# Kernel optimization log

Hardware: AMD Instinct MI355X
Metric: run time of the kernel (lower is better)

Reference implementation:

```python
import jax, jax.numpy as jnp
import numpy as np

D_IN, D_OUT, HEADS, D_K = 256, 256, 8, 32
B, N, L = 2, 128, 512
SCALING = 1.0 / np.sqrt(D_K)


def setup_inputs() -> dict:
    key = jax.random.key(0)
    ks = jax.random.split(key, 12)
    s = 0.02
    return {
        "query": jax.random.normal(ks[0], (B, L, D_IN), jnp.float32),
        "key": jax.random.normal(ks[1], (B, L, D_IN), jnp.float32),
        "value": jax.random.normal(ks[2], (B, N, L, D_OUT), jnp.float32),
        "mask": jax.random.uniform(ks[3], (B, 1, L, L), jnp.float32),
        "Wq": jax.random.normal(ks[4], (D_IN, HEADS * D_K), jnp.float32) * s,
        "bq": jnp.zeros((HEADS * D_K,), jnp.float32),
        "Wk": jax.random.normal(ks[5], (D_IN, HEADS * D_K), jnp.float32) * s,
        "bk": jnp.zeros((HEADS * D_K,), jnp.float32),
        "Wv": jax.random.normal(ks[6], (D_OUT, D_OUT), jnp.float32) * s,
        "bv": jnp.zeros((D_OUT,), jnp.float32),
        "Wo": jax.random.normal(ks[7], (D_OUT, D_OUT), jnp.float32) * s,
        "bo": jnp.zeros((D_OUT,), jnp.float32),
    }


def reference(query, key, value, mask, Wq, bq, Wk, bk, Wv, bv, Wo, bo):
    b, n, l = value.shape[:3]
    h, dk = HEADS, D_K
    dh = value.shape[-1] // h  # per-head value dim
    # projections -> per-head layouts
    q = (query @ Wq + bq).reshape(b, l, h, dk).transpose(0, 2, 1, 3)  # bhld
    k = (key @ Wk + bk).reshape(b, l, h, dk).transpose(0, 2, 1, 3)    # bhld
    v = (value @ Wv + bv).reshape(b, n, l, h, dh).transpose(0, 3, 1, 2, 4)  # bhnld
    q = q * SCALING
    scores = jnp.einsum('bhid,bhjd->bhij', q, k)  # (B,H,L,L)
    scores = jnp.where(mask < 0.5, jnp.finfo(scores.dtype).min, scores)
    attn = jax.nn.softmax(scores, axis=-1)
    # dropout omitted (eval mode / deterministic reference)
    out = jnp.einsum('bhij,bhnjd->bhnid', attn, v)  # (B,H,N,L,dh)
    out = out.transpose(0, 2, 3, 1, 4).reshape(b, n, l, h * dh)
    return out @ Wo + bo
```

## Files before the change

kernel.cpp:

```cpp
#include <hip/hip_runtime.h>
#include <hip/hip_bf16.h>
#include <stdint.h>

#define BB 2
#define LL 512
#define DIN 256
#define HH 8
#define DKK 32
#define NN 128
#define DM 256
#define SCALING 0.17677669529663687f

typedef unsigned short u16;
typedef float f32x4 __attribute__((ext_vector_type(4)));
typedef short s16x8 __attribute__((ext_vector_type(8)));

#define MFMA16(a, b, c) __builtin_amdgcn_mfma_f32_16x16x32_bf16((a), (b), (c), 0, 0, 0)

typedef __attribute__((address_space(3))) char lds_char;
typedef const __attribute__((address_space(1))) char glb_char;

__device__ __forceinline__ void gload16(const void* g, void* l) {
    __builtin_amdgcn_global_load_lds((glb_char*)g, (lds_char*)l, 16, 0, 0);
}

__device__ __forceinline__ u16 f2bf(float f) {
    union { float f; uint32_t i; } v; v.f = f;
    uint32_t x = v.i;
    return (u16)((x + 0x7fffu + ((x >> 16) & 1u)) >> 16);
}

__device__ __forceinline__ uint32_t pack2bf(float f0, float f1) {
    union { float f; uint32_t i; } a, b;
    a.f = f0; b.f = f1;
    return __builtin_amdgcn_perm(b.i + 0x8000u, a.i + 0x8000u, 0x07060302u);
}

__device__ __forceinline__ s16x8 ldsfrag(const u16* base, int row, int cb) {
    const char* p = (const char*)base + row * 128 + (cb ^ ((row & 7) << 4));
    return *(const s16x8*)(const void*)p;
}

__global__ __launch_bounds__(256) void prep_weights(
        const float* __restrict__ Wq, const float* __restrict__ Wk,
        const float* __restrict__ Wv, const float* __restrict__ Wo,
        u16* __restrict__ wqt, u16* __restrict__ wkt,
        u16* __restrict__ wvt, u16* __restrict__ wot) {
    int idx = blockIdx.x * 256 + threadIdx.x;
    int which = idx >> 16;
    const float* src = (which == 0) ? Wq : (which == 1) ? Wk : (which == 2) ? Wv : Wo;
    u16* dst = (which == 0) ? wqt : (which == 1) ? wkt : (which == 2) ? wvt : wot;
    int i = idx & 65535;
    int c = i & 255;
    int k = i >> 8;
    dst[(size_t)c * 256 + k] = f2bf(src[(size_t)k * 256 + c]);
}

__global__ __launch_bounds__(256) void qk_proj(
        const float* __restrict__ q_in, const float* __restrict__ k_in,
        const u16* __restrict__ wqt, const float* __restrict__ bq,
        const u16* __restrict__ wkt, const float* __restrict__ bk,
        u16* __restrict__ q_ws, u16* __restrict__ k_ws) {
    int bid = blockIdx.x;
    int isK = bid & 1;
    int r0 = (bid >> 1) * 64;
    const float* src = isK ? k_in : q_in;
    const u16* wt    = isK ? wkt : wqt;
    const float* bias = isK ? bk : bq;
    u16* dst = isK ? k_ws : q_ws;
    float scale = isK ? 1.0f : SCALING;

    int t = threadIdx.x, w = t >> 6, l = t & 63, lr = l & 15, lg = l >> 4;

    f32x4 zero = {0.f, 0.f, 0.f, 0.f};
    f32x4 acc[4][4];
#pragma unroll
    for (int m = 0; m < 4; m++)
#pragma unroll
        for (int cf = 0; cf < 4; cf++) acc[m][cf] = zero;

#pragma unroll
    for (int ks = 0; ks < 8; ks++) {
        s16x8 afr[4];
#pragma unroll
        for (int m = 0; m < 4; m++) {
            const float* p = src + (size_t)(r0 + m * 16 + lr) * DIN + ks * 32 + lg * 8;
            float4 v0 = *(const float4*)p;
            float4 v1 = *(const float4*)(p + 4);
            union { u16 u[8]; s16x8 v; } tmp;
            tmp.u[0] = f2bf(v0.x); tmp.u[1] = f2bf(v0.y);
            tmp.u[2] = f2bf(v0.z); tmp.u[3] = f2bf(v0.w);
            tmp.u[4] = f2bf(v1.x); tmp.u[5] = f2bf(v1.y);
            tmp.u[6] = f2bf(v1.z); tmp.u[7] = f2bf(v1.w);
            afr[m] = tmp.v;
        }
        s16x8 bfrg[4];
#pragma unroll
        for (int cf = 0; cf < 4; cf++)
            bfrg[cf] = *(const s16x8*)(const void*)(wt + (size_t)(w * 64 + cf * 16 + lr) * 256 + ks * 32 + lg * 8);
#pragma unroll
        for (int m = 0; m < 4; m++)
#pragma unroll
            for (int cf = 0; cf < 4; cf++) acc[m][cf] = MFMA16(afr[m], bfrg[cf], acc[m][cf]);
    }

#pragma unroll
    for (int m = 0; m < 4; m++)
#pragma unroll
        for (int cf = 0; cf < 4; cf++) {
            int c = w * 64 + cf * 16 + lr;
            int h = c >> 5, dd = c & 31;
            float bv_ = bias[c];
#pragma unroll
            for (int r = 0; r < 4; r++) {
                int row = r0 + m * 16 + 4 * lg + r;
                int b = row >> 9, li = row & 511;
                dst[(((size_t)(b * HH + h)) * LL + li) * DKK + dd] = f2bf((acc[m][cf][r] + bv_) * scale);
            }
        }
}

__global__ __launch_bounds__(256) void scores_softmax(
        const u16* __restrict__ q_ws, const u16* __restrict__ k_ws,
        const float* __restrict__ mask, u16* __restrict__ attn) {
    int bid = blockIdx.x;
    int it = bid & 15;
    int bh = bid >> 4;
    int b = bh >> 3;
    int i0 = it * 32;

    __shared__ u16 kl[LL][40];
    __shared__ u16 ql[32][40];
    __shared__ float redmx[2][32];
    __shared__ float redsm[2][32];

    int t = threadIdx.x;
    const u16* kbase = k_ws + (size_t)bh * LL * DKK;
#pragma unroll
    for (int x = 0; x < 8; x++) {
        int idx = x * 256 + t;
        int row = idx >> 2, ch = idx & 3;
        *(s16x8*)(void*)(&kl[row][ch * 8]) = *(const s16x8*)(const void*)(kbase + (size_t)row * DKK + ch * 8);
    }
    if (t < 128) {
        const u16* qbase = q_ws + (size_t)bh * LL * DKK + (size_t)i0 * DKK;
        int row = t >> 2, ch = t & 3;
        *(s16x8*)(void*)(&ql[row][ch * 8]) = *(const s16x8*)(const void*)(qbase + (size_t)row * DKK + ch * 8);
    }
    __syncthreads();

    int w = t >> 6, l = t & 63, lr = l & 15, lg = l >> 4;
    int ih = (w & 1) * 16;
    int jh = (w >> 1) * 256;
    int jhalf = w >> 1;

    s16x8 af = *(const s16x8*)(const void*)(&ql[ih + lr][lg * 8]);
    f32x4 zero = {0.f, 0.f, 0.f, 0.f};
    f32x4 acc[16];
#pragma unroll
    for (int cf = 0; cf < 16; cf++) {
        s16x8 bf = *(const s16x8*)(const void*)(&kl[jh + cf * 16 + lr][lg * 8]);
        acc[cf] = MFMA16(af, bf, zero);
    }

    const float* mrow = mask + (size_t)b * LL * LL;
    float attv[16][4];
    float mx[4], sm[4];
#pragma unroll
    for (int r = 0; r < 4; r++) mx[r] = -3.0e38f;
#pragma unroll
    for (int cf = 0; cf < 16; cf++) {
#pragma unroll
        for (int r = 0; r < 4; r++) {
            int irow = i0 + ih + 4 * lg + r;
            int jcol = jh + cf * 16 + lr;
            float mv = mrow[(size_t)irow * LL + jcol];
            float s = (mv < 0.5f) ? -1.0e30f : acc[cf][r];
            attv[cf][r] = s;
            mx[r] = fmaxf(mx[r], s);
        }
    }
#pragma unroll
    for (int d = 1; d < 16; d <<= 1)
#pragma unroll
        for (int r = 0; r < 4; r++) mx[r] = fmaxf(mx[r], __shfl_xor(mx[r], d));
#pragma unroll
    for (int r = 0; r < 4; r++) sm[r] = 0.f;
#pragma unroll
    for (int cf = 0; cf < 16; cf++)
#pragma unroll
        for (int r = 0; r < 4; r++) {
            float p = __expf(attv[cf][r] - mx[r]);
            attv[cf][r] = p;
            sm[r] += p;
        }
#pragma unroll
    for (int d = 1; d < 16; d <<= 1)
#pragma unroll
        for (int r = 0; r < 4; r++) sm[r] += __shfl_xor(sm[r], d);

    if (lr == 0) {
#pragma unroll
        for (int r = 0; r < 4; r++) {
            redmx[jhalf][ih + 4 * lg + r] = mx[r];
            redsm[jhalf][ih + 4 * lg + r] = sm[r];
        }
    }
    __syncthreads();
    float inv[4];
#pragma unroll
    for (int r = 0; r < 4; r++) {
        int row = ih + 4 * lg + r;
        float m0 = redmx[0][row], m1 = redmx[1][row];
        float s0 = redsm[0][row], s1 = redsm[1][row];
        float gm = fmaxf(m0, m1);
        float gs = s0 * __expf(m0 - gm) + s1 * __expf(m1 - gm);
        inv[r] = __expf(mx[r] - gm) / gs;
    }

    u16* abase = attn + (size_t)bh * LL * LL;
#pragma unroll
    for (int cf = 0; cf < 16; cf++)
#pragma unroll
        for (int r = 0; r < 4; r++) {
            int irow = i0 + ih + 4 * lg + r;
            int jcol = jh + cf * 16 + lr;
            abase[(size_t)irow * LL + jcol] = f2bf(attv[cf][r] * inv[r]);
        }
}

__global__ __launch_bounds__(256, 2) void vproj_gemm(
        const float* __restrict__ value, const float* __restrict__ bv,
        const u16* __restrict__ wvt, u16* __restrict__ ut) {
    __shared__ __align__(16) u16 sm[2 * 16384];

    int t = threadIdx.x;
    int nb = gridDim.x;
    int cpx = nb >> 3;
    int swz = (blockIdx.x & 7) * cpx + (blockIdx.x >> 3);
    int ct = swz & 1;
    int jt = (swz >> 1) & 3;
    int bn = swz >> 3;
    int c0 = ct * 128, j0 = jt * 128;

    int w = t >> 6, l = t & 63, lr = l & 15, lg = l >> 4;
    int wr = w >> 1, wc = w & 1;

    const float* vbase = value + ((size_t)bn * LL + j0) * DM;

    int srow = t >> 3;
    int sgc = t & 7;
    f32x4 zero = {0.f, 0.f, 0.f, 0.f};
    f32x4 acc[4][4];
#pragma unroll
    for (int m = 0; m < 4; m++)
#pragma unroll
        for (int nf = 0; nf < 4; nf++) acc[m][nf] = zero;

    auto stageA = [&](int buf, int kk) {
#pragma unroll
        for (int x = 0; x < 4; x++) {
            int row = x * 32 + srow;
            int gs = sgc ^ (row & 7);
            gload16(wvt + (size_t)(c0 + row) * 256 + kk * 64 + gs * 8,
                    (char*)&sm[buf * 16384] + (x * 256 + t) * 16);
        }
    };
    float4 breg[4][2];
    auto loadB = [&](int kk) {
#pragma unroll
        for (int x = 0; x < 4; x++) {
            int row = x * 32 + srow;
            const float* p = vbase + (size_t)row * DM + kk * 64 + sgc * 8;
            breg[x][0] = *(const float4*)p;
            breg[x][1] = *(const float4*)(p + 4);
        }
    };
    auto writeB = [&](int buf) {
#pragma unroll
        for (int x = 0; x < 4; x++) {
            int row = x * 32 + srow;
            uint32_t p0 = pack2bf(breg[x][0].x, breg[x][0].y);
            uint32_t p1 = pack2bf(breg[x][0].z, breg[x][0].w);
            uint32_t p2 = pack2bf(breg[x][1].x, breg[x][1].y);
            uint32_t p3 = pack2bf(breg[x][1].z, breg[x][1].w);
            uint32_t* dst = (uint32_t*)((char*)&sm[buf * 16384 + 8192]
                            + row * 128 + ((sgc * 16) ^ ((row & 7) << 4)));
            dst[0] = p0; dst[1] = p1; dst[2] = p2; dst[3] = p3;
        }
    };

    stageA(0, 0);
    loadB(0);
    writeB(0);
    __syncthreads();
    int cur = 0;
    for (int kk = 0; kk < 4; kk++) {
        if (kk < 3) {
            stageA(cur ^ 1, kk + 1);
            loadB(kk + 1);
        }
        const u16* Ab = &sm[cur * 16384];
        const u16* Bb = &sm[cur * 16384 + 8192];
        s16x8 af[4][2], bf[4][2];
#pragma unroll
        for (int m = 0; m < 4; m++)
#pragma unroll
            for (int ks = 0; ks < 2; ks++)
                af[m][ks] = ldsfrag(Ab, wr * 64 + m * 16 + lr, ks * 64 + lg * 16);
#pragma unroll
        for (int nf = 0; nf < 4; nf++)
#pragma unroll
            for (int ks = 0; ks < 2; ks++)
                bf[nf][ks] = ldsfrag(Bb, wc * 64 + nf * 16 + lr, ks * 64 + lg * 16);
#pragma unroll
        for (int ks = 0; ks < 2; ks++)
#pragma unroll
            for (int m = 0; m < 4; m++)
#pragma unroll
                for (int nf = 0; nf < 4; nf++)
                    acc[m][nf] = MFMA16(af[m][ks], bf[nf][ks], acc[m][nf]);
        if (kk < 3) writeB(cur ^ 1);
        __syncthreads();
        cur ^= 1;
    }

    u16* ubase = ut + (size_t)bn * DM * LL;
#pragma unroll
    for (int m = 0; m < 4; m++) {
#pragma unroll
        for (int rr = 0; rr < 4; rr++) {
            int c = c0 + wr * 64 + m * 16 + 4 * lg + rr;
            float bvv = bv[c];
#pragma unroll
            for (int nf = 0; nf < 4; nf++) {
                int j = j0 + wc * 64 + nf * 16 + lr;
                ubase[(size_t)c * LL + j] = f2bf(acc[m][nf][rr] + bvv);
            }
        }
    }
}

__global__ __launch_bounds__(256, 2) void pv_gemm(
        const u16* __restrict__ attn, const u16* __restrict__ ut,
        u16* __restrict__ Tm, int n0, int nTiles, int Nc) {
    __shared__ __align__(16) u16 sm[2 * 16384];

    int t = threadIdx.x;
    int nb = gridDim.x;
    int cpx = nb >> 3;
    int swz = (blockIdx.x & 7) * cpx + (blockIdx.x >> 3);
    int nct = swz % nTiles;
    int tmp2 = swz / nTiles;
    int it = tmp2 & 3;
    int bh = tmp2 >> 2;
    int b = bh >> 3, h = bh & 7;
    int i0 = it * 128;

    int w = t >> 6, l = t & 63, lr = l & 15, lg = l >> 4;
    int wr = w >> 1, wc = w & 1;

    const u16* arow0 = attn + (size_t)bh * LL * LL + (size_t)i0 * LL;

    f32x4 zero = {0.f, 0.f, 0.f, 0.f};
    f32x4 acc[4][4];
#pragma unroll
    for (int m = 0; m < 4; m++)
#pragma unroll
        for (int nf = 0; nf < 4; nf++) acc[m][nf] = zero;

    auto stage = [&](int buf, int kk) {
#pragma unroll
        for (int x = 0; x < 4; x++) {
            int G = x * 256 + t;
            int row = G >> 3, gc = G & 7;
            int gs = gc ^ (row & 7);
            gload16(arow0 + (size_t)row * LL + kk * 64 + gs * 8,
                    (char*)&sm[buf * 16384] + G * 16);
        }
#pragma unroll
        for (int x = 0; x < 4; x++) {
            int G = x * 256 + t;
            int row = G >> 3, gc = G & 7;
            int gs = gc ^ (row & 7);
            int nc = nct * 128 + row;
            const u16* src = ut + (((size_t)(b * NN + n0 + (nc >> 5))) * DM + h * DKK + (nc & 31)) * LL
                             + kk * 64 + gs * 8;
            gload16(src, (char*)&sm[buf * 16384 + 8192] + G * 16);
        }
    };

    stage(0, 0);
    __syncthreads();
    int cur = 0;
    for (int kk = 0; kk < 8; kk++) {
        if (kk < 7) stage(cur ^ 1, kk + 1);
        const u16* Ab = &sm[cur * 16384];
        const u16* Bb = &sm[cur * 16384 + 8192];
        s16x8 af[4][2], bf[4][2];
#pragma unroll
        for (int m = 0; m < 4; m++)
#pragma unroll
            for (int ks = 0; ks < 2; ks++)
                af[m][ks] = ldsfrag(Ab, wr * 64 + m * 16 + lr, ks * 64 + lg * 16);
#pragma unroll
        for (int nf = 0; nf < 4; nf++)
#pragma unroll
            for (int ks = 0; ks < 2; ks++)
                bf[nf][ks] = ldsfrag(Bb, wc * 64 + nf * 16 + lr, ks * 64 + lg * 16);
#pragma unroll
        for (int ks = 0; ks < 2; ks++)
#pragma unroll
            for (int m = 0; m < 4; m++)
#pragma unroll
                for (int nf = 0; nf < 4; nf++)
                    acc[m][nf] = MFMA16(af[m][ks], bf[nf][ks], acc[m][nf]);
        __syncthreads();
        cur ^= 1;
    }

#pragma unroll
    for (int m = 0; m < 4; m++) {
        int i = i0 + wr * 64 + m * 16 + 4 * lg;
#pragma unroll
        for (int nf = 0; nf < 4; nf++) {
            int nc = nct * 128 + wc * 64 + nf * 16 + lr;
            int nl = nc >> 5, cl = nc & 31;
            u16* dst = Tm + (((size_t)(b * Nc + nl)) * LL + i) * DM + h * DKK + cl;
#pragma unroll
            for (int rr = 0; rr < 4; rr++)
                dst[(size_t)rr * DM] = f2bf(acc[m][nf][rr]);
        }
    }
}

__global__ __launch_bounds__(256, 2) void wo_gemm(
        const u16* __restrict__ Tm, const u16* __restrict__ wot,
        const float* __restrict__ bo, float* __restrict__ out,
        int n0, int Nc, int nshift) {
    __shared__ __align__(16) u16 sm[2 * 16384];

    int t = threadIdx.x;
    int nb = gridDim.x;
    int cpx = nb >> 3;
    int swz = (blockIdx.x & 7) * cpx + (blockIdx.x >> 3);
    int oc = swz & 1;
    int mt = swz >> 1;
    int r0 = mt * 128;

    int w = t >> 6, l = t & 63, lr = l & 15, lg = l >> 4;
    int wr = w >> 1, wc = w & 1;

    f32x4 zero = {0.f, 0.f, 0.f, 0.f};
    f32x4 acc[4][4];
#pragma unroll
    for (int m = 0; m < 4; m++)
#pragma unroll
        for (int nf = 0; nf < 4; nf++) acc[m][nf] = zero;

    auto stage = [&](int buf, int kk) {
#pragma unroll
        for (int x = 0; x < 4; x++) {
            int G = x * 256 + t;
            int row = G >> 3, gc = G & 7;
            int gs = gc ^ (row & 7);
            gload16(Tm + (size_t)(r0 + row) * DM + kk * 64 + gs * 8,
                    (char*)&sm[buf * 16384] + G * 16);
        }
#pragma unroll
        for (int x = 0; x < 4; x++) {
            int G = x * 256 + t;
            int row = G >> 3, gc = G & 7;
            int gs = gc ^ (row & 7);
            gload16(wot + (size_t)(oc * 128 + row) * DM + kk * 64 + gs * 8,
                    (char*)&sm[buf * 16384 + 8192] + G * 16);
        }
    };

    stage(0, 0);
    __syncthreads();
    int cur = 0;
    for (int kk = 0; kk < 4; kk++) {
        if (kk < 3) stage(cur ^ 1, kk + 1);
        const u16* Ab = &sm[cur * 16384];
        const u16* Bb = &sm[cur * 16384 + 8192];
        s16x8 af[4][2], bf[4][2];
#pragma unroll
        for (int m = 0; m < 4; m++)
#pragma unroll
            for (int ks = 0; ks < 2; ks++)
                af[m][ks] = ldsfrag(Ab, wr * 64 + m * 16 + lr, ks * 64 + lg * 16);
#pragma unroll
        for (int nf = 0; nf < 4; nf++)
#pragma unroll
            for (int ks = 0; ks < 2; ks++)
                bf[nf][ks] = ldsfrag(Bb, wc * 64 + nf * 16 + lr, ks * 64 + lg * 16);
#pragma unroll
        for (int ks = 0; ks < 2; ks++)
#pragma unroll
            for (int m = 0; m < 4; m++)
#pragma unroll
                for (int nf = 0; nf < 4; nf++)
                    acc[m][nf] = MFMA16(af[m][ks], bf[nf][ks], acc[m][nf]);
        __syncthreads();
        cur ^= 1;
    }

#pragma unroll
    for (int nf = 0; nf < 4; nf++) {
        int ocol = oc * 128 + wc * 64 + nf * 16 + lr;
        float bov = bo[ocol];
#pragma unroll
        for (int m = 0; m < 4; m++) {
            int rbase = r0 + wr * 64 + m * 16 + 4 * lg;
#pragma unroll
            for (int rr = 0; rr < 4; rr++) {
                int r = rbase + rr;
                int bnl = r >> 9, i = r & 511;
                int b = bnl >> nshift, nl = bnl & (Nc - 1);
                out[(((size_t)(b * NN + n0 + nl)) * LL + i) * DM + ocol] = acc[m][nf][rr] + bov;
            }
        }
    }
}

extern "C" void kernel_launch(void* const* d_in, const int* in_sizes, int n_in,
                              void* d_out, int out_size, void* d_ws, size_t ws_size,
                              hipStream_t stream) {
    const float* query = (const float*)d_in[0];
    const float* key_  = (const float*)d_in[1];
    const float* value = (const float*)d_in[2];
    const float* mask  = (const float*)d_in[3];
    const float* Wq = (const float*)d_in[4];
    const float* bq = (const float*)d_in[5];
    const float* Wk = (const float*)d_in[6];
    const float* bk = (const float*)d_in[7];
    const float* Wv = (const float*)d_in[8];
    const float* bv = (const float*)d_in[9];
    const float* Wo = (const float*)d_in[10];
    const float* bo = (const float*)d_in[11];

    char* ws = (char*)d_ws;
    u16* wvt  = (u16*)(ws + 0);
    u16* wot  = (u16*)(ws + 131072);
    u16* qw   = (u16*)(ws + 262144);
    u16* kw   = (u16*)(ws + 786432);
    u16* attn = (u16*)(ws + 1310720);
    u16* wqt  = (u16*)(ws + 1310720);
    u16* wkt  = (u16*)(ws + 1310720 + 131072);
    u16* ut   = (u16*)(ws + 9699328);
    u16* Tm   = (u16*)(ws + 76808192);
    float* out = (float*)d_out;

    size_t avail = (ws_size > 76808192u) ? (ws_size - 76808192u) : 0;
    int Nc = 128;
    while (Nc > 4 && (size_t)Nc * 524288u > avail) Nc >>= 1;
    int nshift = 0;
    while ((1 << nshift) < Nc) nshift++;

    hipLaunchKernelGGL(prep_weights,   dim3(1024), dim3(256), 0, stream, Wq, Wk, Wv, Wo, wqt, wkt, wvt, wot);
    hipLaunchKernelGGL(qk_proj,        dim3(32),   dim3(256), 0, stream, query, key_, wqt, bq, wkt, bk, qw, kw);
    hipLaunchKernelGGL(scores_softmax, dim3(256),  dim3(256), 0, stream, qw, kw, mask, attn);
    hipLaunchKernelGGL(vproj_gemm,     dim3(2048), dim3(256), 0, stream, value, bv, wvt, ut);

    int nTiles = Nc >> 2;
    for (int n0 = 0; n0 < NN; n0 += Nc) {
        hipLaunchKernelGGL(pv_gemm, dim3(16 * 4 * nTiles), dim3(256), 0, stream,
                           attn, ut, Tm, n0, nTiles, Nc);
        hipLaunchKernelGGL(wo_gemm, dim3((BB * Nc * LL / 128) * 2), dim3(256), 0, stream,
                           Tm, wot, bo, out, n0, Nc, nshift);
    }
}
```

Before: 185.9 us.

## Stream fp32 value tiles into LDS asynchronously and convert to bf16 at fragment load

```diff
diff --git a/kernel.cpp b/kernel.cpp
--- a/kernel.cpp
+++ b/kernel.cpp
@@ -229,10 +229,11 @@
         }
 }
 
-__global__ __launch_bounds__(256, 2) void vproj_gemm(
+__global__ __launch_bounds__(256, 3) void vproj_gemm(
         const float* __restrict__ value, const float* __restrict__ bv,
         const u16* __restrict__ wvt, u16* __restrict__ ut) {
-    __shared__ __align__(16) u16 sm[2 * 16384];
+    __shared__ __align__(16) u16 smA[2 * 4096];
+    __shared__ __align__(16) float smB[2 * 4096];
 
     int t = threadIdx.x;
     int nb = gridDim.x;
@@ -248,8 +249,6 @@
 
     const float* vbase = value + ((size_t)bn * LL + j0) * DM;
 
-    int srow = t >> 3;
-    int sgc = t & 7;
     f32x4 zero = {0.f, 0.f, 0.f, 0.f};
     f32x4 acc[4][4];
 #pragma unroll
@@ -259,68 +258,59 @@
 
     auto stageA = [&](int buf, int kk) {
 #pragma unroll
+        for (int x = 0; x < 2; x++) {
+            int G = x * 256 + t;
+            int row = G >> 2, gc = G & 3;
+            int gs = gc ^ (row & 3);
+            gload16(wvt + (size_t)(c0 + row) * 256 + kk * 32 + gs * 8,
+                    (char*)&smA[buf * 4096] + G * 16);
+        }
+    };
+    auto stageB = [&](int buf, int kk) {
+#pragma unroll
         for (int x = 0; x < 4; x++) {
-            int row = x * 32 + srow;
-            int gs = sgc ^ (row & 7);
-            gload16(wvt + (size_t)(c0 + row) * 256 + kk * 64 + gs * 8,
-                    (char*)&sm[buf * 16384] + (x * 256 + t) * 16);
+            int G = x * 256 + t;
+            int row = G >> 3, gc = G & 7;
+            int gs = gc ^ (row & 7);
+            gload16(vbase + (size_t)row * DM + kk * 32 + gs * 4,
+                    (char*)&smB[buf * 4096] + G * 16);
         }
     };
-    float4 breg[4][2];
-    auto loadB = [&](int kk) {
-#pragma unroll
-        for (int x = 0; x < 4; x++) {
-            int row = x * 32 + srow;
-            const float* p = vbase + (size_t)row * DM + kk * 64 + sgc * 8;
-            breg[x][0] = *(const float4*)p;
-            breg[x][1] = *(const float4*)(p + 4);
-        }
-    };
-    auto writeB = [&](int buf) {
-#pragma unroll
-        for (int x = 0; x < 4; x++) {
-            int row = x * 32 + srow;
-            uint32_t p0 = pack2bf(breg[x][0].x, breg[x][0].y);
-            uint32_t p1 = pack2bf(breg[x][0].z, breg[x][0].w);
-            uint32_t p2 = pack2bf(breg[x][1].x, breg[x][1].y);
-            uint32_t p3 = pack2bf(breg[x][1].z, breg[x][1].w);
-            uint32_t* dst = (uint32_t*)((char*)&sm[buf * 16384 + 8192]
-                            + row * 128 + ((sgc * 16) ^ ((row & 7) << 4)));
-            dst[0] = p0; dst[1] = p1; dst[2] = p2; dst[3] = p3;
-        }
-    };
 
     stageA(0, 0);
-    loadB(0);
-    writeB(0);
+    stageB(0, 0);
     __syncthreads();
     int cur = 0;
-    for (int kk = 0; kk < 4; kk++) {
-        if (kk < 3) {
-            stageA(cur ^ 1, kk + 1);
-            loadB(kk + 1);
-        }
-        const u16* Ab = &sm[cur * 16384];
-        const u16* Bb = &sm[cur * 16384 + 8192];
-        s16x8 af[4][2], bf[4][2];
+    for (int kk = 0; kk < 8; kk++) {
+        if (kk < 7) { stageA(cur ^ 1, kk + 1); stageB(cur ^ 1, kk + 1); }
+        s16x8 af[4];
+#pragma unroll
+        for (int m = 0; m < 4; m++) {
+            int row = wr * 64 + m * 16 + lr;
+            const char* p = (const char*)&smA[cur * 4096] + row * 64
+                          + ((lg ^ (row & 3)) << 4);
+            af[m] = *(const s16x8*)(const void*)p;
+        }
+        s16x8 bf[4];
+#pragma unroll
+        for (int nf = 0; nf < 4; nf++) {
+            int row = wc * 64 + nf * 16 + lr;
+            int s = row & 7;
+            const char* bp = (const char*)&smB[cur * 4096] + row * 128;
+            f32x4 b0 = *(const f32x4*)(const void*)(bp + (((2 * lg) ^ s) << 4));
+            f32x4 b1 = *(const f32x4*)(const void*)(bp + (((2 * lg + 1) ^ s) << 4));
+            union { uint32_t u[4]; s16x8 v; } tmp;
+            tmp.u[0] = pack2bf(b0[0], b0[1]);
+            tmp.u[1] = pack2bf(b0[2], b0[3]);
+            tmp.u[2] = pack2bf(b1[0], b1[1]);
+            tmp.u[3] = pack2bf(b1[2], b1[3]);
+            bf[nf] = tmp.v;
+        }
 #pragma unroll
         for (int m = 0; m < 4; m++)
 #pragma unroll
-            for (int ks = 0; ks < 2; ks++)
-                af[m][ks] = ldsfrag(Ab, wr * 64 + m * 16 + lr, ks * 64 + lg * 16);
-#pragma unroll
-        for (int nf = 0; nf < 4; nf++)
-#pragma unroll
-            for (int ks = 0; ks < 2; ks++)
-                bf[nf][ks] = ldsfrag(Bb, wc * 64 + nf * 16 + lr, ks * 64 + lg * 16);
-#pragma unroll
-        for (int ks = 0; ks < 2; ks++)
-#pragma unroll
-            for (int m = 0; m < 4; m++)
-#pragma unroll
-                for (int nf = 0; nf < 4; nf++)
-                    acc[m][nf] = MFMA16(af[m][ks], bf[nf][ks], acc[m][nf]);
-        if (kk < 3) writeB(cur ^ 1);
+            for (int nf = 0; nf < 4; nf++)
+                acc[m][nf] = MFMA16(af[m], bf[nf], acc[m][nf]);
         __syncthreads();
         cur ^= 1;
     }
```

New measurement: 188.2 us. No clear change (+1.2%).
